# Kernel optimization log

Measured on AMD Instinct MI355X. Metric: run time of the kernel, lower is better.

The kernel has to match this reference:

```python
import jax, jax.numpy as jnp
import numpy as np

CUTOFF = [2000, 10000, 50000]
INPUT_DIM = 1024
PROJECT_DIMS = [256, 64]  # input_dim / 4, input_dim / 16


def gelu(x):
    # exact erf-based GELU, as in the source
    return x * 0.5 * (1.0 + jax.lax.erf(x / jnp.sqrt(2.0).astype(x.dtype)))


def _ce(logits, labels):
    # sparse softmax cross entropy per row
    lp = jax.nn.log_softmax(logits, axis=-1)
    return -jnp.take_along_axis(lp, labels[:, None], axis=1)[:, 0]


def setup_inputs() -> dict:
    key = jax.random.key(0)
    ks = jax.random.split(key, 10)
    N = 4096
    head_dim = CUTOFF[0] + (len(CUTOFF) - 1)  # 2002
    s = 0.02
    inp = {
        "inputs": jax.random.normal(ks[0], (N, INPUT_DIM), jnp.float32),
        "labels": jax.random.randint(ks[1], (N,), 0, CUTOFF[-1], jnp.int64),
        "head_proj": jax.random.normal(ks[2], (INPUT_DIM, INPUT_DIM), jnp.float32) * s,
        "head_w": jax.random.normal(ks[3], (INPUT_DIM, head_dim), jnp.float32) * s,
        "head_b": jnp.zeros((head_dim,), jnp.float32),
        "tail1_proj_w": jax.random.normal(ks[4], (INPUT_DIM, PROJECT_DIMS[0]), jnp.float32) * s,
        "tail1_w": jax.random.normal(ks[5], (PROJECT_DIMS[0], CUTOFF[1] - CUTOFF[0]), jnp.float32) * s,
        "tail1_b": jnp.zeros((CUTOFF[1] - CUTOFF[0],), jnp.float32),
        "tail2_proj_w": jax.random.normal(ks[6], (INPUT_DIM, PROJECT_DIMS[1]), jnp.float32) * s,
        "tail2_w": jax.random.normal(ks[7], (PROJECT_DIMS[1], CUTOFF[2] - CUTOFF[1]), jnp.float32) * s,
        "tail2_b": jnp.zeros((CUTOFF[2] - CUTOFF[1],), jnp.float32),
    }
    return inp


def reference(inputs, labels, head_proj, head_w, head_b,
              tail1_proj_w, tail1_w, tail1_b,
              tail2_proj_w, tail2_w, tail2_b):
    # Adaptive softmax negative log-likelihood, per token ([N]).
    # Instead of boolean_mask gather / SparseTensor scatter (dynamic shapes),
    # compute per-cluster CE densely and mask — identical math where mask holds.
    tails = [(tail1_proj_w, tail1_w, tail1_b), (tail2_proj_w, tail2_w, tail2_b)]
    head_labels = labels
    loss = jnp.zeros(labels.shape, jnp.float32)
    for i, (pw, w, b) in enumerate(tails):
        lo, hi = CUTOFF[i], CUTOFF[i + 1]
        mask = (labels >= lo) & (labels < hi)
        head_labels = jnp.where(mask, CUTOFF[0] + i, head_labels)
        tail_logits = gelu(inputs @ pw) @ w + b  # [N, hi-lo]
        tail_lab = jnp.clip(labels - lo, 0, hi - lo - 1)
        loss = loss + jnp.where(mask, _ce(tail_logits, tail_lab), 0.0)
    head_logits = gelu(inputs @ head_proj) @ head_w + head_b  # [N, cutoff0+2]
    loss = loss + _ce(head_logits, head_labels)
    return loss
```

## Files before the change

### kernel.cpp

```cpp
#include <hip/hip_runtime.h>
#include <hip/hip_bf16.h>
#include <math.h>

#define NTOK 4096
#define DIM  1024
#define LOG2E 1.4426950408889634f
#define LN2F  0.6931471805599453f

typedef __attribute__((ext_vector_type(8))) short short8;
typedef __attribute__((ext_vector_type(4))) float f32x4;

__device__ __forceinline__ short f2bf(float f) {
    return __builtin_bit_cast(short, __float2bfloat16(f));
}
__device__ __forceinline__ float bf2f(short s) {
    unsigned u = ((unsigned)(unsigned short)s) << 16;
    return __builtin_bit_cast(float, u);
}
__device__ __forceinline__ float gelu_exact(float x) {
    return x * 0.5f * (1.0f + erff(x * 0.70710678118654752f));
}

__device__ __forceinline__
void transpose_tile(const float* __restrict__ src, short* __restrict__ dst,
                    int K, int V, int Vpad, int vt, int kt, float scale)
{
    __shared__ float tile[32][33];
    const int v0 = vt * 32, k0 = kt * 32;
    const int tx = threadIdx.x & 31, ty = threadIdx.x >> 5;
    #pragma unroll
    for (int i = 0; i < 4; ++i) {
        const int k = k0 + ty + 8 * i, v = v0 + tx;
        tile[ty + 8 * i][tx] = (k < K && v < V) ? src[(size_t)k * V + v] : 0.f;
    }
    __syncthreads();
    #pragma unroll
    for (int i = 0; i < 4; ++i) {
        const int v = v0 + ty + 8 * i, k = k0 + tx;
        if (v < Vpad && k < K) dst[(size_t)v * K + k] = f2bf(tile[tx][ty + 8 * i] * scale);
    }
}

__global__ __launch_bounds__(256)
void prep_kernel(const float* __restrict__ X, short* __restrict__ Xb,
                 const float* __restrict__ hp,  short* __restrict__ WhpT,
                 const float* __restrict__ t1p, short* __restrict__ W1pT,
                 const float* __restrict__ t2p, short* __restrict__ W2pT,
                 const float* __restrict__ hw,  short* __restrict__ WhT,
                 const float* __restrict__ t1w, short* __restrict__ W1T,
                 const float* __restrict__ t2w, short* __restrict__ W2T,
                 const int* __restrict__ labels,
                 int* __restrict__ idx1, int* __restrict__ idx2,
                 int* __restrict__ counts)
{
    int b = blockIdx.x;
    if (b < 2048) {
        const size_t idx = ((size_t)b * 256 + threadIdx.x) * 8;
        const float4 a = *reinterpret_cast<const float4*>(X + idx);
        const float4 c = *reinterpret_cast<const float4*>(X + idx + 4);
        short8 v;
        v[0] = f2bf(a.x); v[1] = f2bf(a.y); v[2] = f2bf(a.z); v[3] = f2bf(a.w);
        v[4] = f2bf(c.x); v[5] = f2bf(c.y); v[6] = f2bf(c.z); v[7] = f2bf(c.w);
        *reinterpret_cast<short8*>(Xb + idx) = v;
        return;
    }
    b -= 2048;
    if (b < 1024) { transpose_tile(hp,  WhpT, 1024, 1024,  1024,  b % 32,   b / 32,   1.0f);  return; }
    b -= 1024;
    if (b < 256)  { transpose_tile(t1p, W1pT, 1024, 256,   256,   b % 8,    b / 8,    1.0f);  return; }
    b -= 256;
    if (b < 64)   { transpose_tile(t2p, W2pT, 1024, 64,    64,    b % 2,    b / 2,    1.0f);  return; }
    b -= 64;
    if (b < 2048) { transpose_tile(hw,  WhT,  1024, 2002,  2048,  b % 64,   b / 64,   LOG2E); return; }
    b -= 2048;
    if (b < 2048) { transpose_tile(t1w, W1T,  256,  8000,  8192,  b % 256,  b / 256,  LOG2E); return; }
    b -= 2048;
    if (b < 2560) { transpose_tile(t2w, W2T,  64,  40000,  40960, b % 1280, b / 1280, LOG2E); return; }
    b -= 2560;
    {
        const int i = b * 256 + threadIdx.x;
        const int lab = labels[i];
        if (lab >= 2000 && lab < 10000) idx1[atomicAdd(&counts[0], 1)] = i;
        else if (lab >= 10000)          idx2[atomicAdd(&counts[1], 1)] = i;
    }
}

__global__ __launch_bounds__(512, 2)
void proj5(const short* __restrict__ Xb,
           const short* __restrict__ WhpT, const short* __restrict__ W1pT,
           const short* __restrict__ W2pT,
           short* __restrict__ H, short* __restrict__ T1, short* __restrict__ T2)
{
    constexpr int KSTEP = 256, CHB = 32 * KSTEP * 2;
    __shared__ char sA[2][CHB];
    const int tid = threadIdx.x, w = tid >> 6, l = tid & 63;
    const int arow = l & 15, kg = l >> 4;
    const int c_g = (blockIdx.y * 8 + w) * 16;
    const short* Bt; short* Pout; int Vout, cl; bool active = true;
    if (c_g < 1024)      { Bt = WhpT; Pout = H;  Vout = 1024; cl = c_g; }
    else if (c_g < 1280) { Bt = W1pT; Pout = T1; Vout = 256;  cl = c_g - 1024; }
    else if (c_g < 1344) { Bt = W2pT; Pout = T2; Vout = 64;   cl = c_g - 1280; }
    else                 { Bt = W2pT; Pout = T2; Vout = 64;   cl = 0; active = false; }

    short8 breg[32];
    const short* bp = Bt + (size_t)(cl + arow) * DIM + kg * 8;
    #pragma unroll
    for (int f = 0; f < 32; ++f) breg[f] = *reinterpret_cast<const short8*>(bp + f * 32);

    const int g0 = blockIdx.x * 128;
    short8 st8[2];
    auto load_chunk = [&](int rt, int kh) {
        #pragma unroll
        for (int j = 0; j < 2; ++j) {
            const int v = tid + j * 512;
            const int m = v >> 5, c8 = v & 31;
            st8[j] = *reinterpret_cast<const short8*>(
                Xb + (size_t)(g0 + rt * 32 + m) * DIM + kh * KSTEP + c8 * 8);
        }
    };
    auto store_chunk = [&](int buf) {
        char* base = &sA[buf][0];
        #pragma unroll
        for (int j = 0; j < 2; ++j) {
            const int v = tid + j * 512;
            const int m = v >> 5, c8 = v & 31;
            *reinterpret_cast<short8*>(
                base + (((m * KSTEP + c8 * 8) * 2) ^ ((m & 7) << 4))) = st8[j];
        }
    };

    load_chunk(0, 0); store_chunk(0); __syncthreads();
    f32x4 acc[2] = {(f32x4){0.f,0.f,0.f,0.f}, (f32x4){0.f,0.f,0.f,0.f}};
    for (int rt = 0; rt < 4; ++rt) {
        #pragma unroll
        for (int kh = 0; kh < 4; ++kh) {
            const int buf = kh & 1;
            const bool last = (rt == 3) && (kh == 3);
            if (!last) load_chunk(kh < 3 ? rt : rt + 1, (kh + 1) & 3);
            const char* base = &sA[buf][0];
            #pragma unroll
            for (int f = 0; f < 8; ++f) {
                const short8 af0 = *reinterpret_cast<const short8*>(
                    base + (((arow * KSTEP + f * 32 + kg * 8) * 2) ^ ((arow & 7) << 4)));
                const short8 af1 = *reinterpret_cast<const short8*>(
                    base + ((((16 + arow) * KSTEP + f * 32 + kg * 8) * 2) ^ ((arow & 7) << 4)));
                acc[0] = __builtin_amdgcn_mfma_f32_16x16x32_bf16(af0, breg[kh * 8 + f], acc[0], 0, 0, 0);
                acc[1] = __builtin_amdgcn_mfma_f32_16x16x32_bf16(af1, breg[kh * 8 + f], acc[1], 0, 0, 0);
            }
            if (kh == 3) {
                if (active) {
                    #pragma unroll
                    for (int mr = 0; mr < 2; ++mr)
                        #pragma unroll
                        for (int r = 0; r < 4; ++r)
                            Pout[(size_t)(g0 + rt * 32 + mr * 16 + kg * 4 + r) * Vout + cl + arow] =
                                f2bf(gelu_exact(acc[mr][r]));
                }
                acc[0] = (f32x4){0.f,0.f,0.f,0.f};
                acc[1] = (f32x4){0.f,0.f,0.f,0.f};
            }
            if (!last) store_chunk(buf ^ 1);
            __syncthreads();
        }
    }
}

template<int K, int NT, bool IDENT, int RPG>
__device__ __forceinline__
void ce_core(const short* __restrict__ A, const short* __restrict__ Bt,
             const float* __restrict__ bias, const int* __restrict__ rows,
             const int* __restrict__ countp, float* __restrict__ sum_acc,
             int V, int bx, int by,
             char* __restrict__ sA, float* __restrict__ lsum, int* __restrict__ rlds)
{
    constexpr int KSTEP = (K > 256) ? 256 : K;
    constexpr int NKH   = K / KSTEP;
    constexpr int NKFS  = KSTEP / 32;
    constexpr int NKF   = K / 32;
    constexpr int CHB   = 32 * KSTEP * 2;
    constexpr int NV8   = 32 * KSTEP / 8;
    constexpr int VPT   = (NV8 + 511) / 512;

    const int cnt = IDENT ? NTOK : *countp;
    const int g0 = bx * RPG;
    if (g0 >= cnt) return;
    const int ng = min(RPG, cnt - g0);
    const int tid = threadIdx.x;
    const int w = tid >> 6, l = tid & 63;
    const int arow = l & 15, kg = l >> 4;

    for (int t = tid; t < RPG; t += 512) {
        lsum[t] = 0.f;
        rlds[t] = IDENT ? (g0 + t) : rows[min(g0 + t, cnt - 1)];
    }

    int ct[NT]; float cb[NT]; short8 breg[NT][NKF];
    #pragma unroll
    for (int t = 0; t < NT; ++t) {
        ct[t] = (by * 8 + w) * (16 * NT) + t * 16;
        const int col = ct[t] + arow;
        cb[t] = (col < V) ? __expf(bias[col]) : 0.f;
        const short* bp = Bt + (size_t)(ct[t] + arow) * K + kg * 8;
        #pragma unroll
        for (int f = 0; f < NKF; ++f)
            breg[t][f] = *reinterpret_cast<const short8*>(bp + f * 32);
    }
    __syncthreads();

    const int NRT = (ng + 31) / 32;

    short8 st8[VPT];
    auto load_chunk = [&](int c) {
        const int rt = c / NKH, kh = c % NKH, rb = rt * 32;
        #pragma unroll
        for (int j = 0; j < VPT; ++j) {
            const int v = tid + j * 512;
            if (v < NV8) {
                const int m = v / (KSTEP / 8), c8 = v % (KSTEP / 8);
                st8[j] = *reinterpret_cast<const short8*>(
                    A + (size_t)rlds[min(rb + m, RPG - 1)] * K + kh * KSTEP + c8 * 8);
            }
        }
    };
    auto store_chunk = [&](int buf) {
        char* base = sA + buf * CHB;
        #pragma unroll
        for (int j = 0; j < VPT; ++j) {
            const int v = tid + j * 512;
            if (v < NV8) {
                const int m = v / (KSTEP / 8), c8 = v % (KSTEP / 8);
                *reinterpret_cast<short8*>(
                    base + (((m * KSTEP + c8 * 8) * 2) ^ ((m & 7) << 4))) = st8[j];
            }
        }
    };

    load_chunk(0); store_chunk(0); __syncthreads();

    f32x4 acc[2][NT];
    #pragma unroll
    for (int mr = 0; mr < 2; ++mr)
        #pragma unroll
        for (int t = 0; t < NT; ++t) acc[mr][t] = (f32x4){0.f,0.f,0.f,0.f};

    for (int rt = 0; rt < NRT; ++rt) {
        #pragma unroll
        for (int kh = 0; kh < NKH; ++kh) {
            const int c   = rt * NKH + kh;
            const int buf = (NKH > 1) ? (kh & 1) : (rt & 1);
            const bool last = (c + 1 == NRT * NKH);
            if (!last) load_chunk(c + 1);
            const char* base = sA + buf * CHB;
            #pragma unroll
            for (int f = 0; f < NKFS; ++f) {
                const short8 af0 = *reinterpret_cast<const short8*>(
                    base + (((arow * KSTEP + f * 32 + kg * 8) * 2) ^ ((arow & 7) << 4)));
                const short8 af1 = *reinterpret_cast<const short8*>(
                    base + ((((16 + arow) * KSTEP + f * 32 + kg * 8) * 2) ^ ((arow & 7) << 4)));
                #pragma unroll
                for (int t = 0; t < NT; ++t) {
                    acc[0][t] = __builtin_amdgcn_mfma_f32_16x16x32_bf16(
                        af0, breg[t][kh * NKFS + f], acc[0][t], 0, 0, 0);
                    acc[1][t] = __builtin_amdgcn_mfma_f32_16x16x32_bf16(
                        af1, breg[t][kh * NKFS + f], acc[1][t], 0, 0, 0);
                }
            }
            if (kh == NKH - 1) {
                const int rb = rt * 32;
                #pragma unroll
                for (int mr = 0; mr < 2; ++mr) {
                    float sacc[4] = {0.f, 0.f, 0.f, 0.f};
                    #pragma unroll
                    for (int t = 0; t < NT; ++t)
                        #pragma unroll
                        for (int r = 0; r < 4; ++r)
                            sacc[r] = fmaf(exp2f(acc[mr][t][r]), cb[t], sacc[r]);
                    #pragma unroll
                    for (int r = 0; r < 4; ++r) {
                        float v = sacc[r];
                        v += __shfl_xor(v, 1); v += __shfl_xor(v, 2);
                        v += __shfl_xor(v, 4); v += __shfl_xor(v, 8);
                        if (arow == 0) atomicAdd(&lsum[rb + mr * 16 + kg * 4 + r], v);
                    }
                    #pragma unroll
                    for (int t = 0; t < NT; ++t) acc[mr][t] = (f32x4){0.f,0.f,0.f,0.f};
                }
            }
            if (!last) store_chunk(buf ^ 1);
            __syncthreads();
        }
    }
    for (int t = tid; t < ng; t += 512)
        atomicAdd(&sum_acc[rlds[t]], lsum[t]);
}

template<int RT>
__device__ __forceinline__
void load_a64(const short* __restrict__ A, const int (&rid)[4][2], int kg,
              short8 (&dst)[2][2])
{
    #pragma unroll
    for (int mr = 0; mr < 2; ++mr) {
        const short* ap = A + (size_t)rid[RT][mr] * 64 + kg * 8;
        dst[mr][0] = *reinterpret_cast<const short8*>(ap);
        dst[mr][1] = *reinterpret_cast<const short8*>(ap + 32);
    }
}

__device__ __forceinline__
void ce_reg64(const short* __restrict__ A, const short* __restrict__ Bt,
              const float* __restrict__ bias, const int* __restrict__ rows,
              const int* __restrict__ countp, float* __restrict__ sum_acc,
              int V, int bx, int by, float* __restrict__ lsum)
{
    constexpr int NT = 4, RPG = 128;
    const int cnt = *countp;
    const int g0 = bx * RPG;
    if (g0 >= cnt) return;
    const int ng = min(RPG, cnt - g0);
    const int tid = threadIdx.x;
    const int w = tid >> 6, l = tid & 63;
    const int arow = l & 15, kg = l >> 4;

    for (int t = tid; t < RPG; t += 512) lsum[t] = 0.f;

    int rid[4][2];
    #pragma unroll
    for (int rt = 0; rt < 4; ++rt)
        #pragma unroll
        for (int mr = 0; mr < 2; ++mr)
            rid[rt][mr] = rows[min(g0 + rt * 32 + mr * 16 + arow, cnt - 1)];

    int ct[NT]; float cb[NT]; short8 breg[NT][2];
    #pragma unroll
    for (int t = 0; t < NT; ++t) {
        ct[t] = (by * 8 + w) * 64 + t * 16;
        const int col = ct[t] + arow;
        cb[t] = (col < V) ? __expf(bias[col]) : 0.f;
        const short* bp = Bt + (size_t)(ct[t] + arow) * 64 + kg * 8;
        breg[t][0] = *reinterpret_cast<const short8*>(bp);
        breg[t][1] = *reinterpret_cast<const short8*>(bp + 32);
    }
    __syncthreads();

    auto compute_tile = [&](int rt, const short8 (&Ar)[2][2]) {
        f32x4 acc[2][NT];
        #pragma unroll
        for (int mr = 0; mr < 2; ++mr)
            #pragma unroll
            for (int t = 0; t < NT; ++t) acc[mr][t] = (f32x4){0.f,0.f,0.f,0.f};
        #pragma unroll
        for (int f = 0; f < 2; ++f)
            #pragma unroll
            for (int mr = 0; mr < 2; ++mr)
                #pragma unroll
                for (int t = 0; t < NT; ++t)
                    acc[mr][t] = __builtin_amdgcn_mfma_f32_16x16x32_bf16(
                        Ar[mr][f], breg[t][f], acc[mr][t], 0, 0, 0);
        const int rb = rt * 32;
        #pragma unroll
        for (int mr = 0; mr < 2; ++mr) {
            float sacc[4] = {0.f, 0.f, 0.f, 0.f};
            #pragma unroll
            for (int t = 0; t < NT; ++t)
                #pragma unroll
                for (int r = 0; r < 4; ++r)
                    sacc[r] = fmaf(exp2f(acc[mr][t][r]), cb[t], sacc[r]);
            #pragma unroll
            for (int r = 0; r < 4; ++r) {
                float v = sacc[r];
                v += __shfl_xor(v, 1); v += __shfl_xor(v, 2);
                v += __shfl_xor(v, 4); v += __shfl_xor(v, 8);
                if (arow == 0) atomicAdd(&lsum[rb + mr * 16 + kg * 4 + r], v);
            }
        }
    };

    short8 A0[2][2], A1[2][2];
    load_a64<0>(A, rid, kg, A0);
    load_a64<1>(A, rid, kg, A1);
    compute_tile(0, A0);
    load_a64<2>(A, rid, kg, A0);
    compute_tile(1, A1);
    load_a64<3>(A, rid, kg, A1);
    compute_tile(2, A0);
    compute_tile(3, A1);

    __syncthreads();
    for (int t = tid; t < ng; t += 512)
        atomicAdd(&sum_acc[rows[g0 + t]], lsum[t]);
}

__global__ __launch_bounds__(512, 2)
void ce_head(const short* __restrict__ H, const short* __restrict__ WhT,
             const float* __restrict__ head_b, float* __restrict__ hsum)
{
    __shared__ char  sA[2][16384];
    __shared__ float lsum[128];
    __shared__ int   rlds[128];
    ce_core<1024, 1, true, 128>(H, WhT, head_b, nullptr, nullptr, hsum, 2002,
                                blockIdx.x, blockIdx.y, &sA[0][0], lsum, rlds);
}

#define NB_T2 2560
__global__ __launch_bounds__(512, 4)
void ce_tails(const short* __restrict__ T1, const short* __restrict__ W1T,
              const float* __restrict__ t1b,
              const short* __restrict__ T2, const short* __restrict__ W2T,
              const float* __restrict__ t2b,
              const int* __restrict__ idx1, const int* __restrict__ idx2,
              const int* __restrict__ counts, float* __restrict__ tsum)
{
    __shared__ char  sA[2][16384];
    __shared__ float lsum[128];
    __shared__ int   rlds[128];
    const int b = blockIdx.x;
    if (b < NB_T2) {
        ce_reg64(T2, W2T, t2b, idx2, &counts[1], tsum, 40000,
                 b / 80, b % 80, lsum);
    } else {
        const int b2 = b - NB_T2;
        ce_core<256, 2, false, 128>(T1, W1T, t1b, idx1, &counts[0], tsum, 8000,
                                    b2 / 32, b2 % 32, &sA[0][0], lsum, rlds);
    }
}

__global__ __launch_bounds__(256)
void finalize_kernel(const int* __restrict__ labels,
                     const short* __restrict__ H,  const short* __restrict__ WhT,
                     const float* __restrict__ head_b,
                     const short* __restrict__ T1, const short* __restrict__ W1T,
                     const float* __restrict__ t1b,
                     const short* __restrict__ T2, const short* __restrict__ W2T,
                     const float* __restrict__ t2b,
                     const float* __restrict__ hsum, const float* __restrict__ tsum,
                     float* __restrict__ out)
{
    const int r = blockIdx.x * 4 + (threadIdx.x >> 6);
    const int l = threadIdx.x & 63;
    if (r >= NTOK) return;
    const int lab = labels[r];
    int labH = lab;
    if (lab >= 10000) labH = 2001; else if (lab >= 2000) labH = 2000;

    float d = 0.f;
    {
        const short* a = H   + (size_t)r    * 1024 + l * 16;
        const short* b = WhT + (size_t)labH * 1024 + l * 16;
        #pragma unroll
        for (int u = 0; u < 2; ++u) {
            const short8 av = *reinterpret_cast<const short8*>(a + u * 8);
            const short8 bv = *reinterpret_cast<const short8*>(b + u * 8);
            #pragma unroll
            for (int e = 0; e < 8; ++e) d = fmaf(bf2f(av[e]), bf2f(bv[e]), d);
        }
    }
    float td = 0.f;
    if (lab >= 2000) {
        const short* a; const short* b; int nl;
        if (lab < 10000) { a = T1 + (size_t)r * 256; b = W1T + (size_t)(lab - 2000) * 256; nl = 32; }
        else             { a = T2 + (size_t)r * 64;  b = W2T + (size_t)(lab - 10000) * 64; nl = 8; }
        if (l < nl) {
            const short8 av = *reinterpret_cast<const short8*>(a + l * 8);
            const short8 bv = *reinterpret_cast<const short8*>(b + l * 8);
            #pragma unroll
            for (int e = 0; e < 8; ++e) td = fmaf(bf2f(av[e]), bf2f(bv[e]), td);
        }
    }
    #pragma unroll
    for (int off = 32; off; off >>= 1) { d += __shfl_xor(d, off); td += __shfl_xor(td, off); }
    if (l == 0) {
        float loss = logf(hsum[r]) - (d * LN2F + head_b[labH]);
        if (lab >= 2000) {
            const float tb = (lab < 10000) ? t1b[lab - 2000] : t2b[lab - 10000];
            loss += logf(tsum[r]) - (td * LN2F + tb);
        }
        out[r] = loss;
    }
}

extern "C" void kernel_launch(void* const* d_in, const int* in_sizes, int n_in,
                              void* d_out, int out_size, void* d_ws, size_t ws_size,
                              hipStream_t stream) {
    (void)in_sizes; (void)n_in; (void)out_size; (void)ws_size;
    const float* X         = (const float*)d_in[0];
    const int*   labels    = (const int*)  d_in[1];
    const float* head_proj = (const float*)d_in[2];
    const float* head_w    = (const float*)d_in[3];
    const float* head_b    = (const float*)d_in[4];
    const float* t1p       = (const float*)d_in[5];
    const float* t1w       = (const float*)d_in[6];
    const float* t1b       = (const float*)d_in[7];
    const float* t2p       = (const float*)d_in[8];
    const float* t2w       = (const float*)d_in[9];
    const float* t2b       = (const float*)d_in[10];
    float* out = (float*)d_out;

    char* ws = (char*)d_ws;
    int*   counts = (int*)ws;
    int*   idx1   = (int*)(ws + 1024);
    int*   idx2   = (int*)(ws + 1024 + 16384);
    float* hsum   = (float*)(ws + 65536);
    float* tsum   = hsum + NTOK;

    short* p = (short*)(ws + 131072);
    short* Xb   = p; p += (size_t)NTOK * 1024;
    short* WhpT = p; p += (size_t)1024 * 1024;
    short* W1pT = p; p += (size_t)256  * 1024;
    short* W2pT = p; p += (size_t)64   * 1024;
    short* WhT  = p; p += (size_t)2048 * 1024;
    short* W1T  = p; p += (size_t)8192 * 256;
    short* W2T  = p; p += (size_t)40960 * 64;
    short* H    = p; p += (size_t)NTOK * 1024;
    short* T1   = p; p += (size_t)NTOK * 256;
    short* T2   = p; p += (size_t)NTOK * 64;

    hipMemsetAsync(counts, 0, 16, stream);
    hipMemsetAsync(hsum, 0, 2 * NTOK * sizeof(float), stream);

    prep_kernel<<<10064, 256, 0, stream>>>(X, Xb, head_proj, WhpT, t1p, W1pT,
                                           t2p, W2pT, head_w, WhT, t1w, W1T, t2w, W2T,
                                           labels, idx1, idx2, counts);
    proj5<<<dim3(32, 11), 512, 0, stream>>>(Xb, WhpT, W1pT, W2pT, H, T1, T2);

    ce_head<<<dim3(32, 16), 512, 0, stream>>>(H, WhT, head_b, hsum);
    ce_tails<<<NB_T2 + 256, 512, 0, stream>>>(T1, W1T, t1b, T2, W2T, t2b,
                                              idx1, idx2, counts, tsum);

    finalize_kernel<<<NTOK / 4, 256, 0, stream>>>(
        labels, H, WhT, head_b, T1, W1T, t1b, T2, W2T, t2b, hsum, tsum, out);
}
```

Measured before the change: 199.5 us.

## Double rows per tail-2 CE block and drop log2e prescaling of logit weights

The tail-2 cross-entropy kernel now processes 256 gathered rows per block instead of 128, which halves the block count. Row indices are staged in shared memory and a software-pipelined loop runs over 8 row tiles, so each block reuses its register-resident weight fragments across twice as many rows. Separately, the LOG2E scaling of the weights in prep is removed and exp2f becomes __expf, with finalize no longer multiplying by ln2. The trade-off is fewer blocks to spread across CUs and a possible small precision change from the different exponential path.

```diff
diff --git a/kernel.cpp b/kernel.cpp
--- a/kernel.cpp
+++ b/kernel.cpp
@@ -4,8 +4,6 @@
 
 #define NTOK 4096
 #define DIM  1024
-#define LOG2E 1.4426950408889634f
-#define LN2F  0.6931471805599453f
 
 typedef __attribute__((ext_vector_type(8))) short short8;
 typedef __attribute__((ext_vector_type(4))) float f32x4;
@@ -23,7 +21,7 @@
 
 __device__ __forceinline__
 void transpose_tile(const float* __restrict__ src, short* __restrict__ dst,
-                    int K, int V, int Vpad, int vt, int kt, float scale)
+                    int K, int V, int Vpad, int vt, int kt)
 {
     __shared__ float tile[32][33];
     const int v0 = vt * 32, k0 = kt * 32;
@@ -37,7 +35,7 @@
     #pragma unroll
     for (int i = 0; i < 4; ++i) {
         const int v = v0 + ty + 8 * i, k = k0 + tx;
-        if (v < Vpad && k < K) dst[(size_t)v * K + k] = f2bf(tile[tx][ty + 8 * i] * scale);
+        if (v < Vpad && k < K) dst[(size_t)v * K + k] = f2bf(tile[tx][ty + 8 * i]);
     }
 }
 
@@ -65,17 +63,17 @@
         return;
     }
     b -= 2048;
-    if (b < 1024) { transpose_tile(hp,  WhpT, 1024, 1024,  1024,  b % 32,   b / 32,   1.0f);  return; }
+    if (b < 1024) { transpose_tile(hp,  WhpT, 1024, 1024,  1024,  b % 32,   b / 32);   return; }
     b -= 1024;
-    if (b < 256)  { transpose_tile(t1p, W1pT, 1024, 256,   256,   b % 8,    b / 8,    1.0f);  return; }
+    if (b < 256)  { transpose_tile(t1p, W1pT, 1024, 256,   256,   b % 8,    b / 8);    return; }
     b -= 256;
-    if (b < 64)   { transpose_tile(t2p, W2pT, 1024, 64,    64,    b % 2,    b / 2,    1.0f);  return; }
+    if (b < 64)   { transpose_tile(t2p, W2pT, 1024, 64,    64,    b % 2,    b / 2);    return; }
     b -= 64;
-    if (b < 2048) { transpose_tile(hw,  WhT,  1024, 2002,  2048,  b % 64,   b / 64,   LOG2E); return; }
+    if (b < 2048) { transpose_tile(hw,  WhT,  1024, 2002,  2048,  b % 64,   b / 64);   return; }
     b -= 2048;
-    if (b < 2048) { transpose_tile(t1w, W1T,  256,  8000,  8192,  b % 256,  b / 256,  LOG2E); return; }
+    if (b < 2048) { transpose_tile(t1w, W1T,  256,  8000,  8192,  b % 256,  b / 256);  return; }
     b -= 2048;
-    if (b < 2560) { transpose_tile(t2w, W2T,  64,  40000,  40960, b % 1280, b / 1280, LOG2E); return; }
+    if (b < 2560) { transpose_tile(t2w, W2T,  64,  40000,  40960, b % 1280, b / 1280); return; }
     b -= 2560;
     {
         const int i = b * 256 + threadIdx.x;
@@ -274,7 +272,7 @@
                     for (int t = 0; t < NT; ++t)
                         #pragma unroll
                         for (int r = 0; r < 4; ++r)
-                            sacc[r] = fmaf(exp2f(acc[mr][t][r]), cb[t], sacc[r]);
+                            sacc[r] = fmaf(__expf(acc[mr][t][r]), cb[t], sacc[r]);
                     #pragma unroll
                     for (int r = 0; r < 4; ++r) {
                         float v = sacc[r];
@@ -294,26 +292,14 @@
         atomicAdd(&sum_acc[rlds[t]], lsum[t]);
 }
 
-template<int RT>
-__device__ __forceinline__
-void load_a64(const short* __restrict__ A, const int (&rid)[4][2], int kg,
-              short8 (&dst)[2][2])
-{
-    #pragma unroll
-    for (int mr = 0; mr < 2; ++mr) {
-        const short* ap = A + (size_t)rid[RT][mr] * 64 + kg * 8;
-        dst[mr][0] = *reinterpret_cast<const short8*>(ap);
-        dst[mr][1] = *reinterpret_cast<const short8*>(ap + 32);
-    }
-}
-
 __device__ __forceinline__
 void ce_reg64(const short* __restrict__ A, const short* __restrict__ Bt,
               const float* __restrict__ bias, const int* __restrict__ rows,
               const int* __restrict__ countp, float* __restrict__ sum_acc,
-              int V, int bx, int by, float* __restrict__ lsum)
-{
-    constexpr int NT = 4, RPG = 128;
+              int V, int bx, int by,
+              float* __restrict__ lsum, int* __restrict__ rlds)
+{
+    constexpr int NT = 4, RPG = 256;
     const int cnt = *countp;
     const int g0 = bx * RPG;
     if (g0 >= cnt) return;
@@ -322,14 +308,10 @@
     const int w = tid >> 6, l = tid & 63;
     const int arow = l & 15, kg = l >> 4;
 
-    for (int t = tid; t < RPG; t += 512) lsum[t] = 0.f;
-
-    int rid[4][2];
-    #pragma unroll
-    for (int rt = 0; rt < 4; ++rt)
-        #pragma unroll
-        for (int mr = 0; mr < 2; ++mr)
-            rid[rt][mr] = rows[min(g0 + rt * 32 + mr * 16 + arow, cnt - 1)];
+    for (int t = tid; t < RPG; t += 512) {
+        lsum[t] = 0.f;
+        rlds[t] = rows[min(g0 + t, cnt - 1)];
+    }
 
     int ct[NT]; float cb[NT]; short8 breg[NT][2];
     #pragma unroll
@@ -343,6 +325,15 @@
     }
     __syncthreads();
 
+    auto load_tile = [&](int rt, short8 (&dst)[2][2]) {
+        #pragma unroll
+        for (int mr = 0; mr < 2; ++mr) {
+            const int r = rlds[rt * 32 + mr * 16 + arow];
+            const short* ap = A + (size_t)r * 64 + kg * 8;
+            dst[mr][0] = *reinterpret_cast<const short8*>(ap);
+            dst[mr][1] = *reinterpret_cast<const short8*>(ap + 32);
+        }
+    };
     auto compute_tile = [&](int rt, const short8 (&Ar)[2][2]) {
         f32x4 acc[2][NT];
         #pragma unroll
@@ -365,7 +356,7 @@
             for (int t = 0; t < NT; ++t)
                 #pragma unroll
                 for (int r = 0; r < 4; ++r)
-                    sacc[r] = fmaf(exp2f(acc[mr][t][r]), cb[t], sacc[r]);
+                    sacc[r] = fmaf(__expf(acc[mr][t][r]), cb[t], sacc[r]);
             #pragma unroll
             for (int r = 0; r < 4; ++r) {
                 float v = sacc[r];
@@ -377,18 +368,19 @@
     };
 
     short8 A0[2][2], A1[2][2];
-    load_a64<0>(A, rid, kg, A0);
-    load_a64<1>(A, rid, kg, A1);
-    compute_tile(0, A0);
-    load_a64<2>(A, rid, kg, A0);
-    compute_tile(1, A1);
-    load_a64<3>(A, rid, kg, A1);
-    compute_tile(2, A0);
-    compute_tile(3, A1);
+    load_tile(0, A0);
+    load_tile(1, A1);
+    #pragma unroll
+    for (int rt = 0; rt < 8; rt += 2) {
+        compute_tile(rt, A0);
+        if (rt + 2 < 8) load_tile(rt + 2, A0);
+        compute_tile(rt + 1, A1);
+        if (rt + 3 < 8) load_tile(rt + 3, A1);
+    }
 
     __syncthreads();
     for (int t = tid; t < ng; t += 512)
-        atomicAdd(&sum_acc[rows[g0 + t]], lsum[t]);
+        atomicAdd(&sum_acc[rlds[t]], lsum[t]);
 }
 
 __global__ __launch_bounds__(512, 2)
@@ -402,7 +394,7 @@
                                 blockIdx.x, blockIdx.y, &sA[0][0], lsum, rlds);
 }
 
-#define NB_T2 2560
+#define NB_T2 1280
 __global__ __launch_bounds__(512, 4)
 void ce_tails(const short* __restrict__ T1, const short* __restrict__ W1T,
               const float* __restrict__ t1b,
@@ -412,12 +404,12 @@
               const int* __restrict__ counts, float* __restrict__ tsum)
 {
     __shared__ char  sA[2][16384];
-    __shared__ float lsum[128];
-    __shared__ int   rlds[128];
+    __shared__ float lsum[256];
+    __shared__ int   rlds[256];
     const int b = blockIdx.x;
     if (b < NB_T2) {
         ce_reg64(T2, W2T, t2b, idx2, &counts[1], tsum, 40000,
-                 b / 80, b % 80, lsum);
+                 b / 80, b % 80, lsum, rlds);
     } else {
         const int b2 = b - NB_T2;
         ce_core<256, 2, false, 128>(T1, W1T, t1b, idx1, &counts[0], tsum, 8000,
@@ -470,10 +462,10 @@
     #pragma unroll
     for (int off = 32; off; off >>= 1) { d += __shfl_xor(d, off); td += __shfl_xor(td, off); }
     if (l == 0) {
-        float loss = logf(hsum[r]) - (d * LN2F + head_b[labH]);
+        float loss = logf(hsum[r]) - (d + head_b[labH]);
         if (lab >= 2000) {
             const float tb = (lab < 10000) ? t1b[lab - 2000] : t2b[lab - 10000];
-            loss += logf(tsum[r]) - (td * LN2F + tb);
+            loss += logf(tsum[r]) - (td + tb);
         }
         out[r] = loss;
     }
```

Result: faster. 185.6 us (-7.0%).
